# Optimization experiments

Hardware: AMD Instinct MI355X
Metric: run time of the kernel (lower is better)

Reference implementation:

```python
import jax, jax.numpy as jnp
import numpy as np

NC = 80
REG_MAX = 16
NO = REG_MAX * 4 + NC  # 144
LEVEL_SHAPES = [(80, 80), (40, 40), (20, 20)]
STRIDES = [8.0, 16.0, 32.0]
CHANNELS = [256, 512, 512]


def _make_anchors():
    """Returns anchor_points (2, A) and stride_tensor (1, A), grid offset 0.5."""
    pts, sts = [], []
    for (h, w), s in zip(LEVEL_SHAPES, STRIDES):
        sx = jnp.arange(w, dtype=jnp.float32) + 0.5
        sy = jnp.arange(h, dtype=jnp.float32) + 0.5
        gy, gx = jnp.meshgrid(sy, sx, indexing='ij')
        pts.append(jnp.stack([gx.ravel(), gy.ravel()], axis=-1))  # (h*w, 2)
        sts.append(jnp.full((h * w,), s, dtype=jnp.float32))
    anchors = jnp.concatenate(pts, axis=0).T          # (2, A)
    strides = jnp.concatenate(sts, axis=0)[None, :]   # (1, A)
    return anchors, strides


def setup_inputs() -> dict:
    key = jax.random.key(0)
    ks = jax.random.split(key, 16)
    inp = {}
    inp['x0'] = jax.random.normal(ks[0], (16, 256, 80, 80), dtype=jnp.float32)
    inp['x1'] = jax.random.normal(ks[1], (16, 512, 40, 40), dtype=jnp.float32)
    inp['x2'] = jax.random.normal(ks[2], (16, 512, 20, 20), dtype=jnp.float32)
    # per-level 1x1 conv head weights: box branch (4*reg_max out), cls branch (nc out)
    for i, c in enumerate(CHANNELS):
        sc = 1.0 / np.sqrt(c)
        inp[f'w_box{i}'] = jax.random.normal(ks[3 + 4 * i], (REG_MAX * 4, c), dtype=jnp.float32) * sc
        inp[f'b_box{i}'] = jax.random.normal(ks[4 + 4 * i], (REG_MAX * 4,), dtype=jnp.float32) * 0.01
        inp[f'w_cls{i}'] = jax.random.normal(ks[5 + 4 * i], (NC, c), dtype=jnp.float32) * sc
        inp[f'b_cls{i}'] = jax.random.normal(ks[6 + 4 * i], (NC,), dtype=jnp.float32) * 0.01
    return inp


def _level_out(x, wb, bb, wc, bc):
    # cat(cv2(x), cv3(x), dim=1) then view(B, no, -1)
    box = jnp.einsum('bchw,oc->bohw', x, wb) + bb[None, :, None, None]
    cls = jnp.einsum('bchw,oc->bohw', x, wc) + bc[None, :, None, None]
    B = x.shape[0]
    return jnp.concatenate([box, cls], axis=1).reshape(B, NO, -1)


def reference(x0, x1, x2,
              w_box0, b_box0, w_cls0, b_cls0,
              w_box1, b_box1, w_cls1, b_cls1,
              w_box2, b_box2, w_cls2, b_cls2):
    xs = [x0, x1, x2]
    wbs = [w_box0, w_box1, w_box2]
    bbs = [b_box0, b_box1, b_box2]
    wcs = [w_cls0, w_cls1, w_cls2]
    bcs = [b_cls0, b_cls1, b_cls2]
    x_cat = jnp.concatenate(
        [_level_out(x, wb, bb, wc, bc) for x, wb, bb, wc, bc in zip(xs, wbs, bbs, wcs, bcs)],
        axis=2)  # (B, 144, A)
    B, _, A = x_cat.shape
    box, cls = x_cat[:, :REG_MAX * 4, :], x_cat[:, REG_MAX * 4:, :]

    # DFL: (B, 4*16, A) -> softmax over 16 bins -> expected distance per side
    p = jax.nn.softmax(box.reshape(B, 4, REG_MAX, A), axis=2)
    dist = jnp.einsum('bkra,r->bka', p, jnp.arange(REG_MAX, dtype=jnp.float32))  # (B, 4, A)

    # dist2bbox (xywh) on anchor grid, scale by stride
    anchors, strides = _make_anchors()
    anc = anchors[None]                 # (1, 2, A)
    lt, rb = dist[:, :2, :], dist[:, 2:, :]
    x1y1 = anc - lt
    x2y2 = anc + rb
    c_xy = (x1y1 + x2y2) * 0.5
    wh = x2y2 - x1y1
    dbox = jnp.concatenate([c_xy, wh], axis=1) * strides[:, None, :]  # (B, 4, A)

    # boxes (B, A, 4), scores (B, A, nc) -- the tensors fed to EfficientNMS_TRT
    boxes = jnp.transpose(dbox, (0, 2, 1))
    scores = jnp.transpose(cls, (0, 2, 1))
    return jnp.concatenate([boxes, scores], axis=-1)  # (B, A, 4 + nc)
```

## Files before the change

kernel.cpp:

```cpp
#include <hip/hip_runtime.h>


typedef __bf16 bf16x8 __attribute__((ext_vector_type(8)));
typedef float  f32x4  __attribute__((ext_vector_type(4)));

#define NTHREADS 256

#define WOFF0 0
#define WOFF1 73728
#define WOFF2 221184
#define WCHUNK_BYTES 18432

__device__ __forceinline__ unsigned int pack_bf16(float a, float b) {
    unsigned int ua = __builtin_bit_cast(unsigned int, a);
    unsigned int ub = __builtin_bit_cast(unsigned int, b);
    return ((ua + 0x8000u) >> 16) | ((ub + 0x8000u) & 0xffff0000u);
}

__device__ __forceinline__ int swz(int row, int kbyte) {
    return row * 128 + (kbyte ^ ((row & 7) << 4));
}

__device__ __forceinline__ void gload_lds16(const void* g, void* l) {
    __builtin_amdgcn_global_load_lds(
        (const __attribute__((address_space(1))) void*)g,
        (__attribute__((address_space(3))) void*)l, 16, 0, 0);
}

__global__ __launch_bounds__(256)
void prep_w_kernel(const float* __restrict__ wb0, const float* __restrict__ wc0,
                   const float* __restrict__ wb1, const float* __restrict__ wc1,
                   const float* __restrict__ wb2, const float* __restrict__ wc2,
                   unsigned char* __restrict__ ws) {
    int uid = blockIdx.x * 256 + threadIdx.x;
    if (uid >= 23040) return;
    const float* wb; const float* wc; int C; size_t off; int uu;
    if (uid < 4608)       { wb = wb0; wc = wc0; C = 256; off = WOFF0; uu = uid; }
    else if (uid < 13824) { wb = wb1; wc = wc1; C = 512; off = WOFF1; uu = uid - 4608; }
    else                  { wb = wb2; wc = wc2; C = 512; off = WOFF2; uu = uid - 13824; }
    const int kunits = C / 8;
    const int row = uu / kunits;
    const int k   = (uu % kunits) * 8;
    const float* src = ((row < 64) ? (wb + row * C) : (wc + (row - 64) * C)) + k;
    const float4 f0 = *(const float4*)(src);
    const float4 f1 = *(const float4*)(src + 4);
    uint4 p;
    p.x = pack_bf16(f0.x, f0.y);
    p.y = pack_bf16(f0.z, f0.w);
    p.z = pack_bf16(f1.x, f1.y);
    p.w = pack_bf16(f1.z, f1.w);
    const int chunk = k >> 6;
    const int kg    = (k & 63) >> 3;
    *(uint4*)(ws + off + (size_t)chunk * WCHUNK_BYTES + swz(row, kg * 16)) = p;
}

template <int LVL>
__device__ __forceinline__ void run_level(
        int rb,
        const float* __restrict__ x,
        const unsigned char* __restrict__ wimg_all,
        const float* __restrict__ bbox, const float* __restrict__ bcls,
        float* __restrict__ out,
        unsigned char* s_w, unsigned char* s_x) {

    constexpr int    C      = (LVL == 0) ? 256 : 512;
    constexpr int    GW     = (LVL == 0) ? 80 : (LVL == 1 ? 40 : 20);
    constexpr int    HW     = GW * GW;
    constexpr int    AOFF   = (LVL == 0) ? 0 : (LVL == 1 ? 6400 : 8000);
    constexpr float  STRIDE = (LVL == 0) ? 8.0f : (LVL == 1 ? 16.0f : 32.0f);
    constexpr int    TPB    = (HW + 63) / 64;
    constexpr size_t WOFF   = (LVL == 0) ? WOFF0 : (LVL == 1 ? WOFF1 : WOFF2);

    const int b    = rb / TPB;
    const int tile = rb % TPB;
    const int hw0  = tile * 64;
    const int nv   = (HW - hw0 < 64) ? (HW - hw0) : 64;

    const int tid  = threadIdx.x;
    const int wv   = tid >> 6;
    const int lane = tid & 63;
    const int col  = lane & 15;
    const int q4   = lane >> 4;

    const float* xb = x + (size_t)b * C * HW;
    const unsigned char* wimg = wimg_all + WOFF;

    const int anc  = lane;
    const int kgb  = wv;
    const int ancc = (anc < nv) ? anc : (nv - 1);
    const float* xcol = xb + hw0 + ancc;

    f32x4 acc[9];
#pragma unroll
    for (int m = 0; m < 9; ++m) acc[m] = (f32x4){0.f, 0.f, 0.f, 0.f};

    float xv[2][8];
#pragma unroll
    for (int i = 0; i < 2; ++i) {
        const float* p = xcol + (size_t)((kgb + 4 * i) * 8) * HW;
#pragma unroll
        for (int j = 0; j < 8; ++j) xv[i][j] = p[(size_t)j * HW];
    }

    const int nkc = C / 64;
    for (int kc = 0; kc < nkc; ++kc) {
        __syncthreads();

#pragma unroll
        for (int i = 0; i < 5; ++i) {
            int u = tid + i * 256;
            if (u < 1152)
                gload_lds16(wimg + (size_t)kc * WCHUNK_BYTES + u * 16, s_w + u * 16);
        }

#pragma unroll
        for (int i = 0; i < 2; ++i) {
            const int kg = kgb + 4 * i;
            uint4 q;
            q.x = pack_bf16(xv[i][0], xv[i][1]);
            q.y = pack_bf16(xv[i][2], xv[i][3]);
            q.z = pack_bf16(xv[i][4], xv[i][5]);
            q.w = pack_bf16(xv[i][6], xv[i][7]);
            *(uint4*)(s_x + swz(anc, kg * 16)) = q;
        }

        __syncthreads();

        if (kc + 1 < nkc) {
            const int k0n = (kc + 1) * 64;
#pragma unroll
            for (int i = 0; i < 2; ++i) {
                const float* p = xcol + (size_t)(k0n + (kgb + 4 * i) * 8) * HW;
#pragma unroll
                for (int j = 0; j < 8; ++j) xv[i][j] = p[(size_t)j * HW];
            }
        }

#pragma unroll
        for (int ks = 0; ks < 2; ++ks) {
            const int kbyte = ks * 64 + q4 * 16;
            const bf16x8 bf = *(const bf16x8*)(s_x + swz(wv * 16 + col, kbyte));
#pragma unroll
            for (int m = 0; m < 9; ++m) {
                const bf16x8 af = *(const bf16x8*)(s_w + swz(m * 16 + col, kbyte));
                acc[m] = __builtin_amdgcn_mfma_f32_16x16x32_bf16(af, bf, acc[m], 0, 0, 0);
            }
        }
    }

    float4 bcv[5];
#pragma unroll
    for (int m = 0; m < 5; ++m)
        bcv[m] = *(const float4*)(bcls + m * 16 + q4 * 4);

    const float LOG2E = 1.44269504088896f;

    const int alocal = wv * 16 + col;
    const bool valid = alocal < nv;
    const int hw = hw0 + alocal;

    float dist[4];
#pragma unroll
    for (int g = 0; g < 4; ++g) {
        const float4 bbv = *(const float4*)(bbox + g * 16 + q4 * 4);
        const float v0 = acc[g][0] + bbv.x;
        const float v1 = acc[g][1] + bbv.y;
        const float v2 = acc[g][2] + bbv.z;
        const float v3 = acc[g][3] + bbv.w;
        float mx = fmaxf(fmaxf(v0, v1), fmaxf(v2, v3));
        mx = fmaxf(mx, __shfl_xor(mx, 16));
        mx = fmaxf(mx, __shfl_xor(mx, 32));
        const float e0 = __builtin_amdgcn_exp2f((v0 - mx) * LOG2E);
        const float e1 = __builtin_amdgcn_exp2f((v1 - mx) * LOG2E);
        const float e2 = __builtin_amdgcn_exp2f((v2 - mx) * LOG2E);
        const float e3 = __builtin_amdgcn_exp2f((v3 - mx) * LOG2E);
        float s  = e0 + e1 + e2 + e3;
        float ws = e1 + 2.f * e2 + 3.f * e3 + (float)(q4 * 4) * s;
        s  += __shfl_xor(s, 16);
        s  += __shfl_xor(s, 32);
        ws += __shfl_xor(ws, 16);
        ws += __shfl_xor(ws, 32);
        dist[g] = ws / s;
    }

    if (valid) {
        const size_t obase = ((size_t)b * 8400 + AOFF + hw) * 84;
        if (q4 == 0) {
            const float ax = (float)(hw % GW) + 0.5f;
            const float ay = (float)(hw / GW) + 0.5f;
            f32x4 bx;
            bx[0] = (ax + 0.5f * (dist[2] - dist[0])) * STRIDE;
            bx[1] = (ay + 0.5f * (dist[3] - dist[1])) * STRIDE;
            bx[2] = (dist[0] + dist[2]) * STRIDE;
            bx[3] = (dist[1] + dist[3]) * STRIDE;
            *(f32x4*)(out + obase) = bx;
        }
#pragma unroll
        for (int m = 0; m < 5; ++m) {
            f32x4 v;
            v[0] = acc[m + 4][0] + bcv[m].x;
            v[1] = acc[m + 4][1] + bcv[m].y;
            v[2] = acc[m + 4][2] + bcv[m].z;
            v[3] = acc[m + 4][3] + bcv[m].w;
            *(f32x4*)(out + obase + 4 + m * 16 + q4 * 4) = v;
        }
    }
}

__global__ __launch_bounds__(NTHREADS, 6)
void UltralyticsDetect_kernel(
        const float* __restrict__ x0, const float* __restrict__ x1, const float* __restrict__ x2,
        const unsigned char* __restrict__ wimg,
        const float* __restrict__ bb0, const float* __restrict__ bc0,
        const float* __restrict__ bb1, const float* __restrict__ bc1,
        const float* __restrict__ bb2, const float* __restrict__ bc2,
        float* __restrict__ out) {

    __shared__ __align__(16) unsigned char s_w[144 * 64 * 2];
    __shared__ __align__(16) unsigned char s_x[64 * 64 * 2];

    const int bid = blockIdx.x;
    if (bid < 400) {
        run_level<1>(bid, x1, wimg, bb1, bc1, out, s_w, s_x);
    } else if (bid < 512) {
        run_level<2>(bid - 400, x2, wimg, bb2, bc2, out, s_w, s_x);
    } else {
        run_level<0>(bid - 512, x0, wimg, bb0, bc0, out, s_w, s_x);
    }
}

extern "C" void kernel_launch(void* const* d_in, const int* in_sizes, int n_in,
                              void* d_out, int out_size, void* d_ws, size_t ws_size,
                              hipStream_t stream) {
    const float* x0  = (const float*)d_in[0];
    const float* x1  = (const float*)d_in[1];
    const float* x2  = (const float*)d_in[2];
    const float* wb0 = (const float*)d_in[3];
    const float* bb0 = (const float*)d_in[4];
    const float* wc0 = (const float*)d_in[5];
    const float* bc0 = (const float*)d_in[6];
    const float* wb1 = (const float*)d_in[7];
    const float* bb1 = (const float*)d_in[8];
    const float* wc1 = (const float*)d_in[9];
    const float* bc1 = (const float*)d_in[10];
    const float* wb2 = (const float*)d_in[11];
    const float* bb2 = (const float*)d_in[12];
    const float* wc2 = (const float*)d_in[13];
    const float* bc2 = (const float*)d_in[14];

    unsigned char* wimg = (unsigned char*)d_ws;

    prep_w_kernel<<<90, 256, 0, stream>>>(wb0, wc0, wb1, wc1, wb2, wc2, wimg);

    UltralyticsDetect_kernel<<<2112, NTHREADS, 0, stream>>>(
        x0, x1, x2, wimg,
        bb0, bc0, bb1, bc1, bb2, bc2,
        (float*)d_out);
}
```

Measured before the change: 55.19 us.

## Double-buffer weight chunks and feed activations directly into MFMA registers

Replaces the single-buffered weight and activation LDS staging with a double-buffered weight ring and per-lane activation loads that go straight into MFMA B-fragments after bf16 packing. The activation tile no longer passes through LDS, and with the ring only one barrier per chunk is needed, governed by explicit vmcnt waits. Activations are prefetched two chunks ahead in register sets P and Q. This adds register pressure, so the launch bound drops from 6 to 4 blocks per CU, which may lower occupancy. It also relies on hand-tuned waitcnt counts being correct.

After: 50.09 us. 9.2% less time.

```diff
diff --git a/kernel.cpp b/kernel.cpp
--- a/kernel.cpp
+++ b/kernel.cpp
@@ -61,7 +61,7 @@
         const unsigned char* __restrict__ wimg_all,
         const float* __restrict__ bbox, const float* __restrict__ bcls,
         float* __restrict__ out,
-        unsigned char* s_w, unsigned char* s_x) {
+        unsigned char* s_w) {
 
     constexpr int    C      = (LVL == 0) ? 256 : 512;
     constexpr int    GW     = (LVL == 0) ? 80 : (LVL == 1 ? 40 : 20);
@@ -70,6 +70,7 @@
     constexpr float  STRIDE = (LVL == 0) ? 8.0f : (LVL == 1 ? 16.0f : 32.0f);
     constexpr int    TPB    = (HW + 63) / 64;
     constexpr size_t WOFF   = (LVL == 0) ? WOFF0 : (LVL == 1 ? WOFF1 : WOFF2);
+    const int nkc = C / 64;
 
     const int b    = rb / TPB;
     const int tile = rb % TPB;
@@ -85,68 +86,93 @@
     const float* xb = x + (size_t)b * C * HW;
     const unsigned char* wimg = wimg_all + WOFF;
 
-    const int anc  = lane;
-    const int kgb  = wv;
-    const int ancc = (anc < nv) ? anc : (nv - 1);
-    const float* xcol = xb + hw0 + ancc;
+    const int alocal = wv * 16 + col;
+    const int ancc   = (alocal < nv) ? alocal : (nv - 1);
+    const float* xanc = xb + hw0 + ancc;
 
     f32x4 acc[9];
 #pragma unroll
     for (int m = 0; m < 9; ++m) acc[m] = (f32x4){0.f, 0.f, 0.f, 0.f};
 
-    float xv[2][8];
-#pragma unroll
-    for (int i = 0; i < 2; ++i) {
-        const float* p = xcol + (size_t)((kgb + 4 * i) * 8) * HW;
-#pragma unroll
-        for (int j = 0; j < 8; ++j) xv[i][j] = p[(size_t)j * HW];
-    }
-
-    const int nkc = C / 64;
-    for (int kc = 0; kc < nkc; ++kc) {
-        __syncthreads();
-
-#pragma unroll
-        for (int i = 0; i < 5; ++i) {
-            int u = tid + i * 256;
-            if (u < 1152)
-                gload_lds16(wimg + (size_t)kc * WCHUNK_BYTES + u * 16, s_w + u * 16);
-        }
-
-#pragma unroll
-        for (int i = 0; i < 2; ++i) {
-            const int kg = kgb + 4 * i;
-            uint4 q;
-            q.x = pack_bf16(xv[i][0], xv[i][1]);
-            q.y = pack_bf16(xv[i][2], xv[i][3]);
-            q.z = pack_bf16(xv[i][4], xv[i][5]);
-            q.w = pack_bf16(xv[i][6], xv[i][7]);
-            *(uint4*)(s_x + swz(anc, kg * 16)) = q;
-        }
-
-        __syncthreads();
-
-        if (kc + 1 < nkc) {
-            const int k0n = (kc + 1) * 64;
-#pragma unroll
-            for (int i = 0; i < 2; ++i) {
-                const float* p = xcol + (size_t)(k0n + (kgb + 4 * i) * 8) * HW;
-#pragma unroll
-                for (int j = 0; j < 8; ++j) xv[i][j] = p[(size_t)j * HW];
-            }
-        }
-
-#pragma unroll
-        for (int ks = 0; ks < 2; ++ks) {
-            const int kbyte = ks * 64 + q4 * 16;
-            const bf16x8 bf = *(const bf16x8*)(s_x + swz(wv * 16 + col, kbyte));
-#pragma unroll
-            for (int m = 0; m < 9; ++m) {
-                const bf16x8 af = *(const bf16x8*)(s_w + swz(m * 16 + col, kbyte));
-                acc[m] = __builtin_amdgcn_mfma_f32_16x16x32_bf16(af, bf, acc[m], 0, 0, 0);
-            }
-        }
-    }
+    float P[16], Q[16];
+
+#define XLOAD(V, CC)                                                        \
+    {                                                                       \
+        const float* _p = xanc + (size_t)((CC) * 64 + q4 * 8) * HW;         \
+        _Pragma("unroll")                                                   \
+        for (int _ks = 0; _ks < 2; ++_ks)                                   \
+            _Pragma("unroll")                                               \
+            for (int _j = 0; _j < 8; ++_j)                                  \
+                V[_ks * 8 + _j] = _p[(size_t)(_ks * 32 + _j) * HW];         \
+    }
+
+#define WDMA(CC, BUF)                                                       \
+    {                                                                       \
+        _Pragma("unroll")                                                   \
+        for (int _i = 0; _i < 5; ++_i) {                                    \
+            int _u = tid + _i * 256;                                        \
+            if (_u < 1152)                                                  \
+                gload_lds16(wimg + (size_t)(CC) * WCHUNK_BYTES + _u * 16,   \
+                            s_w + (BUF) * WCHUNK_BYTES + _u * 16);          \
+        }                                                                   \
+    }
+
+#define CVT(V, KS, DST)                                                     \
+    {                                                                       \
+        uint4 _q;                                                           \
+        _q.x = pack_bf16(V[(KS) * 8 + 0], V[(KS) * 8 + 1]);                 \
+        _q.y = pack_bf16(V[(KS) * 8 + 2], V[(KS) * 8 + 3]);                 \
+        _q.z = pack_bf16(V[(KS) * 8 + 4], V[(KS) * 8 + 5]);                 \
+        _q.w = pack_bf16(V[(KS) * 8 + 6], V[(KS) * 8 + 7]);                 \
+        DST = __builtin_bit_cast(bf16x8, _q);                               \
+    }
+
+#define CHUNK_BODY(KC, V, BUF)                                              \
+    {                                                                       \
+        if ((KC) + 1 < nkc) WDMA((KC) + 1, 1 - (BUF));                      \
+        __builtin_amdgcn_sched_barrier(0);                                  \
+        bf16x8 _f0, _f1;                                                    \
+        CVT(V, 0, _f0);                                                     \
+        CVT(V, 1, _f1);                                                     \
+        const bool _refill = (KC) + 2 < nkc;                                \
+        if (_refill) XLOAD(V, (KC) + 2);                                    \
+        __builtin_amdgcn_sched_barrier(0);                                  \
+        _Pragma("unroll")                                                   \
+        for (int _m = 0; _m < 9; ++_m) {                                    \
+            const bf16x8 _a0 = *(const bf16x8*)(s_w + (BUF) * WCHUNK_BYTES  \
+                                    + swz(_m * 16 + col, q4 * 16));         \
+            acc[_m] = __builtin_amdgcn_mfma_f32_16x16x32_bf16(_a0, _f0,     \
+                                                    acc[_m], 0, 0, 0);      \
+            const bf16x8 _a1 = *(const bf16x8*)(s_w + (BUF) * WCHUNK_BYTES  \
+                                    + swz(_m * 16 + col, 64 + q4 * 16));    \
+            acc[_m] = __builtin_amdgcn_mfma_f32_16x16x32_bf16(_a1, _f1,     \
+                                                    acc[_m], 0, 0, 0);      \
+        }                                                                   \
+        __builtin_amdgcn_sched_barrier(0);                                  \
+        if (_refill) asm volatile("s_waitcnt vmcnt(16)" ::: "memory");      \
+        else         asm volatile("s_waitcnt vmcnt(0)"  ::: "memory");      \
+        __builtin_amdgcn_s_barrier();                                       \
+        __builtin_amdgcn_sched_barrier(0);                                  \
+    }
+
+    WDMA(0, 0);
+    __builtin_amdgcn_sched_barrier(0);
+    XLOAD(P, 0);
+    XLOAD(Q, 1);
+    __builtin_amdgcn_sched_barrier(0);
+    asm volatile("s_waitcnt vmcnt(32)" ::: "memory");
+    __builtin_amdgcn_s_barrier();
+    __builtin_amdgcn_sched_barrier(0);
+
+    for (int kc2 = 0; kc2 < nkc; kc2 += 2) {
+        CHUNK_BODY(kc2,     P, 0);
+        CHUNK_BODY(kc2 + 1, Q, 1);
+    }
+
+#undef CHUNK_BODY
+#undef CVT
+#undef WDMA
+#undef XLOAD
 
     float4 bcv[5];
 #pragma unroll
@@ -155,7 +181,6 @@
 
     const float LOG2E = 1.44269504088896f;
 
-    const int alocal = wv * 16 + col;
     const bool valid = alocal < nv;
     const int hw = hw0 + alocal;
 
@@ -207,7 +232,7 @@
     }
 }
 
-__global__ __launch_bounds__(NTHREADS, 6)
+__global__ __launch_bounds__(NTHREADS, 4)
 void UltralyticsDetect_kernel(
         const float* __restrict__ x0, const float* __restrict__ x1, const float* __restrict__ x2,
         const unsigned char* __restrict__ wimg,
@@ -216,16 +241,15 @@
         const float* __restrict__ bb2, const float* __restrict__ bc2,
         float* __restrict__ out) {
 
-    __shared__ __align__(16) unsigned char s_w[144 * 64 * 2];
-    __shared__ __align__(16) unsigned char s_x[64 * 64 * 2];
+    __shared__ __align__(16) unsigned char s_w[2 * WCHUNK_BYTES];
 
     const int bid = blockIdx.x;
     if (bid < 400) {
-        run_level<1>(bid, x1, wimg, bb1, bc1, out, s_w, s_x);
+        run_level<1>(bid, x1, wimg, bb1, bc1, out, s_w);
     } else if (bid < 512) {
-        run_level<2>(bid - 400, x2, wimg, bb2, bc2, out, s_w, s_x);
+        run_level<2>(bid - 400, x2, wimg, bb2, bc2, out, s_w);
     } else {
-        run_level<0>(bid - 512, x0, wimg, bb0, bc0, out, s_w, s_x);
+        run_level<0>(bid - 512, x0, wimg, bb0, bc0, out, s_w);
     }
 }
 
```
